# Optimization experiments

Measured on AMD Instinct MI355X. Metric: run time of the kernel, lower is better.

Reference implementation:

```python
import jax, jax.numpy as jnp
import numpy as np

B, N, T_OUT, C_IN, D_EMB, C_OUT = 8, 3072, 128, 32, 8, 64
BIG = 1e10


def setup_inputs() -> dict:
    key = jax.random.key(0)
    k = jax.random.split(key, 10)
    # x: (B, N, 3) tuples of (feature_id, value, time)
    f = jax.random.randint(k[0], (B, N), 0, C_IN).astype(jnp.float32)
    v = jax.random.normal(k[1], (B, N), dtype=jnp.float32)
    t = jax.random.uniform(k[2], (B, N), dtype=jnp.float32) * (T_OUT - 1)
    x = jnp.stack([f, v, t], axis=-1)
    out_positions = jnp.arange(T_OUT, dtype=jnp.float32)
    # parameters
    W_dist = jax.random.normal(k[3], (D_EMB,), dtype=jnp.float32) * 0.05   # Linear(1, D) weight
    b_dist = jnp.zeros((D_EMB,), dtype=jnp.float32)
    emb = jax.random.normal(k[4], (C_IN + 1, D_EMB), dtype=jnp.float32) * 0.05  # Embedding(C+1, D)
    W_vals = jax.random.normal(k[5], (D_EMB,), dtype=jnp.float32) * 0.05   # Linear(1, D) weight
    b_vals = jnp.zeros((D_EMB,), dtype=jnp.float32)
    W_lin = jax.random.normal(k[6], (C_OUT, D_EMB * C_IN), dtype=jnp.float32) * 0.05
    b_lin = jnp.zeros((C_OUT,), dtype=jnp.float32)
    kernel_scale = jnp.float32(0.5)
    return {"x": x, "out_positions": out_positions, "W_dist": W_dist, "b_dist": b_dist,
            "emb": emb, "W_vals": W_vals, "b_vals": b_vals, "W_lin": W_lin,
            "b_lin": b_lin, "kernel_scale": kernel_scale}


def reference(x, out_positions, W_dist, b_dist, emb, W_vals, b_vals, W_lin, b_lin, kernel_scale):
    C = emb.shape[0] - 1
    f = x[:, :, 0].astype(jnp.int32)   # (B, N) channel ids
    v = x[:, :, 1]                      # (B, N)
    t = x[:, :, 2]                      # (B, N)
    max_pos = jnp.max(out_positions)

    # --- observation encodings: (B, T, N, D) ---
    dists = (t[:, None, :] - out_positions[None, :, None]) / max_pos  # (B, T, N)
    x_enc = (dists[..., None] * W_dist + b_dist) \
            + emb[f][:, None, :, :] \
            + (v[:, :, None] * W_vals + b_vals)[:, None, :, :]

    # --- kernel inverse-density estimate (kernel_smoothing == 1 -> min), detached ---
    pd = jnp.abs(t[:, :, None] - t[:, None, :])          # (B, N, N)
    same = f[:, :, None] == f[:, None, :]
    pd = jnp.where(same & (pd != 0), pd, BIG)
    inv_density = jax.lax.stop_gradient(jnp.min(pd, axis=1))  # (B, N)

    # --- causal & padding masks ---
    causal = (t[:, None, :] - out_positions[None, :, None]) <= 0  # (B, T, N)
    padding = jnp.any(x != 0, axis=2)[:, None, :]                 # (B, 1, N)
    m = (causal & padding).astype(x.dtype)                        # (B, T, N)

    # --- per-channel density-weighted pooling, vectorized over channels ---
    # (density*mask)**ks == density**ks * mask since density>0 and mask in {0,1}
    dw = inv_density ** kernel_scale                              # (B, N)
    onehot = (f[:, :, None] == jnp.arange(C)).astype(x.dtype)     # (B, N, C)
    Z = jnp.einsum('btn,bn,bnc->btc', m, dw, onehot)              # density normalizer
    cnt = jnp.einsum('btn,bnc->btc', m, onehot)                   # mask count
    wx = x_enc * (m * dw[:, None, :])[..., None]                  # (B, T, N, D)
    num = jnp.einsum('btnd,bnc->btcd', wx, onehot)                # (B, T, C, D)
    fe = num / (Z + 1e-10)[..., None] / (cnt + 1e-10)[..., None]  # (B, T, C, D)

    y = fe.reshape(fe.shape[0], fe.shape[1], -1)                  # concat channels -> (B, T, C*D)
    out = y @ W_lin.T + b_lin                                     # (B, T, C_OUT)
    return jnp.transpose(out, (0, 2, 1))                          # (B, C_OUT, T)
```

## Files before the change

kernel.cpp:

```cpp
#include <hip/hip_runtime.h>
#include <math.h>

#define B 8
#define N 3072
#define T_OUTN 128
#define C_INN 32
#define D_EMBN 8
#define C_OUTN 64
#define BIGF 1e10f

__global__ void k12(const float* __restrict__ x,
                    const float* __restrict__ W_dist, const float* __restrict__ b_dist,
                    const float* __restrict__ emb,    const float* __restrict__ W_vals,
                    const float* __restrict__ b_vals, const float* __restrict__ W_lin,
                    const float* __restrict__ ks_p,
                    float* __restrict__ G, float* __restrict__ U) {
    const int tid = threadIdx.x;
    if (blockIdx.x == B * C_INN) {
        for (int e = tid; e < 3 * C_INN * C_OUTN; e += 256) {
            int comp = e / (C_INN * C_OUTN);
            int rem  = e % (C_INN * C_OUTN);
            int c = rem / C_OUTN;
            int o = rem % C_OUTN;
            float s = 0.f;
            #pragma unroll
            for (int d = 0; d < D_EMBN; ++d) {
                float w = W_lin[o * (C_INN * D_EMBN) + c * D_EMBN + d];
                float g;
                if (comp == 0)      g = W_dist[d];
                else if (comp == 1) g = b_dist[d] + b_vals[d] + emb[c * D_EMBN + d];
                else                g = W_vals[d];
                s += w * g;
            }
            U[e] = s;
        }
        return;
    }

    __shared__ __align__(16) float tl[N + 4];
    __shared__ float vl[N];
    __shared__ float hist[4][T_OUTN];
    __shared__ int cnt_s;

    const int b = blockIdx.x / C_INN;
    const int c = blockIdx.x % C_INN;
    const float* xb = x + (size_t)b * N * 3;

    for (int i = tid; i < 4 * T_OUTN; i += 256) ((float*)hist)[i] = 0.f;
    if (tid == 0) cnt_s = 0;
    __syncthreads();

    for (int idx = tid; idx < N; idx += 256) {
        float fv = xb[idx * 3 + 0];
        if ((int)fv == c) {
            float vv = xb[idx * 3 + 1];
            float tv = xb[idx * 3 + 2];
            int p = atomicAdd(&cnt_s, 1);
            tl[p] = tv;
            vl[p] = vv;
        }
    }
    __syncthreads();
    const int M = cnt_s;
    const int Mpad = (M + 3) & ~3;
    if (tid < Mpad - M) tl[M + tid] = -BIGF;
    __syncthreads();

    const float ks = ks_p[0];
    for (int p = tid; p < M; p += 256) {
        const float tp = tl[p];
        const float vp = vl[p];
        float m = BIGF;
        for (int j = 0; j < Mpad; j += 4) {
            float4 t4 = *(const float4*)&tl[j];
            float d0 = fabsf(t4.x - tp); if (d0 != 0.f) m = fminf(m, d0);
            float d1 = fabsf(t4.y - tp); if (d1 != 0.f) m = fminf(m, d1);
            float d2 = fabsf(t4.z - tp); if (d2 != 0.f) m = fminf(m, d2);
            float d3 = fabsf(t4.w - tp); if (d3 != 0.f) m = fminf(m, d3);
        }
        bool pad = (c == 0) && (tp == 0.f) && (vp == 0.f);
        if (!pad) {
            float w = powf(m, ks);
            int k = (int)ceilf(tp);
            atomicAdd(&hist[0][k], w);
            atomicAdd(&hist[1][k], 1.f);
            atomicAdd(&hist[2][k], w * tp);
            atomicAdd(&hist[3][k], w * vp);
        }
    }
    __syncthreads();

    {
        const int comp = tid >> 6;
        const int lane = tid & 63;
        float a  = hist[comp][2 * lane];
        float bb = hist[comp][2 * lane + 1];
        float s = a + bb;
        #pragma unroll
        for (int off = 1; off < 64; off <<= 1) {
            float t = __shfl_up(s, off);
            if (lane >= off) s += t;
        }
        hist[comp][2 * lane]     = s - bb;
        hist[comp][2 * lane + 1] = s;
    }
    __syncthreads();

    if (tid < T_OUTN) {
        const int tau = tid;
        float Z   = hist[0][tau];
        float cnt = hist[1][tau];
        float St  = hist[2][tau];
        float Sv  = hist[3][tau];
        float inv = 1.f / ((Z + 1e-10f) * (cnt + 1e-10f));
        float g1 = (St - (float)tau * Z) * inv * (1.f / 127.f);
        float g2 = Z * inv;
        float g3 = Sv * inv;
        float* Gb = G + (size_t)(b * C_INN + c) * 3 * T_OUTN;
        Gb[0 * T_OUTN + tau] = g1;
        Gb[1 * T_OUTN + tau] = g2;
        Gb[2 * T_OUTN + tau] = g3;
    }
}

__global__ void k3_out(const float* __restrict__ U, const float* __restrict__ G,
                       const float* __restrict__ b_lin, float* __restrict__ out) {
    __shared__ __align__(16) float Us[3 * C_INN * C_OUTN];
    __shared__ float Gs[4 * 100];
    const int tid = threadIdx.x;
    const int b  = blockIdx.x >> 5;
    const int t0 = (blockIdx.x & 31) * 4;

    for (int i = tid; i < (3 * C_INN * C_OUTN) / 4; i += 256)
        ((float4*)Us)[i] = ((const float4*)U)[i];
    for (int i = tid; i < 4 * C_INN * 3; i += 256) {
        int taul = i / (C_INN * 3);
        int rem  = i % (C_INN * 3);
        int c    = rem / 3;
        int comp = rem % 3;
        Gs[taul * 100 + rem] =
            G[((size_t)(b * C_INN + c) * 3 + comp) * T_OUTN + t0 + taul];
    }
    __syncthreads();

    const int o    = tid >> 2;
    const int taul = tid & 3;
    float acc = b_lin[o];
    #pragma unroll 4
    for (int c = 0; c < C_INN; ++c) {
        float g1 = Gs[taul * 100 + c * 3 + 0];
        float g2 = Gs[taul * 100 + c * 3 + 1];
        float g3 = Gs[taul * 100 + c * 3 + 2];
        acc += Us[0 * C_INN * C_OUTN + c * C_OUTN + o] * g1
             + Us[1 * C_INN * C_OUTN + c * C_OUTN + o] * g2
             + Us[2 * C_INN * C_OUTN + c * C_OUTN + o] * g3;
    }
    out[((size_t)b * C_OUTN + o) * T_OUTN + t0 + taul] = acc;
}

extern "C" void kernel_launch(void* const* d_in, const int* in_sizes, int n_in,
                              void* d_out, int out_size, void* d_ws, size_t ws_size,
                              hipStream_t stream) {
    const float* x      = (const float*)d_in[0];
    const float* W_dist = (const float*)d_in[2];
    const float* b_dist = (const float*)d_in[3];
    const float* emb    = (const float*)d_in[4];
    const float* W_vals = (const float*)d_in[5];
    const float* b_vals = (const float*)d_in[6];
    const float* W_lin  = (const float*)d_in[7];
    const float* b_lin  = (const float*)d_in[8];
    const float* ks     = (const float*)d_in[9];

    float* ws = (float*)d_ws;
    float* U  = ws;
    float* G  = U + 3 * C_INN * C_OUTN;
    float* out = (float*)d_out;

    k12<<<B * C_INN + 1, 256, 0, stream>>>(x, W_dist, b_dist, emb, W_vals,
                                           b_vals, W_lin, ks, G, U);
    k3_out<<<B * (T_OUTN / 4), 256, 0, stream>>>(U, G, b_lin, out);
}
```

Before: 103.2 us.

## Fuse both kernels into one per-batch block with channel-bucketed points

Replaces the two-kernel pipeline (one block per batch×channel, then a separate output projection kernel) with a single kernel of one 1024-thread block per batch. Points are counting-sorted by channel in shared memory, so each point scans only its own channel's bucket for the nearest-time distance. Per-channel histograms, the prefix sums, the projected weights and the final linear layer all stay in LDS, which removes the global workspace round trip and the second launch. The cost is only 8 blocks on a large GPU and heavy LDS use per block, so most CUs sit idle.

```diff
diff --git a/kernel.cpp b/kernel.cpp
--- a/kernel.cpp
+++ b/kernel.cpp
@@ -9,153 +9,131 @@
 #define C_OUTN 64
 #define BIGF 1e10f
 
-__global__ void k12(const float* __restrict__ x,
-                    const float* __restrict__ W_dist, const float* __restrict__ b_dist,
-                    const float* __restrict__ emb,    const float* __restrict__ W_vals,
-                    const float* __restrict__ b_vals, const float* __restrict__ W_lin,
-                    const float* __restrict__ ks_p,
-                    float* __restrict__ G, float* __restrict__ U) {
+__global__ __launch_bounds__(1024) void fused(
+    const float* __restrict__ x,
+    const float* __restrict__ W_dist, const float* __restrict__ b_dist,
+    const float* __restrict__ emb,    const float* __restrict__ W_vals,
+    const float* __restrict__ b_vals, const float* __restrict__ W_lin,
+    const float* __restrict__ b_lin,  const float* __restrict__ ks_p,
+    float* __restrict__ out)
+{
+    __shared__ __align__(16) float tl[N];
+    __shared__ float vl[N];
+    __shared__ int   cl[N];
+    __shared__ float hist[C_INN][4][T_OUTN];
+    __shared__ __align__(16) float Us[3][C_INN][C_OUTN];
+    __shared__ int cnt[C_INN], off[C_INN + 1], place[C_INN];
+
     const int tid = threadIdx.x;
-    if (blockIdx.x == B * C_INN) {
-        for (int e = tid; e < 3 * C_INN * C_OUTN; e += 256) {
-            int comp = e / (C_INN * C_OUTN);
-            int rem  = e % (C_INN * C_OUTN);
-            int c = rem / C_OUTN;
-            int o = rem % C_OUTN;
-            float s = 0.f;
-            #pragma unroll
-            for (int d = 0; d < D_EMBN; ++d) {
-                float w = W_lin[o * (C_INN * D_EMBN) + c * D_EMBN + d];
-                float g;
-                if (comp == 0)      g = W_dist[d];
-                else if (comp == 1) g = b_dist[d] + b_vals[d] + emb[c * D_EMBN + d];
-                else                g = W_vals[d];
-                s += w * g;
-            }
-            U[e] = s;
-        }
-        return;
-    }
-
-    __shared__ __align__(16) float tl[N + 4];
-    __shared__ float vl[N];
-    __shared__ float hist[4][T_OUTN];
-    __shared__ int cnt_s;
-
-    const int b = blockIdx.x / C_INN;
-    const int c = blockIdx.x % C_INN;
+    const int b   = blockIdx.x;
     const float* xb = x + (size_t)b * N * 3;
 
-    for (int i = tid; i < 4 * T_OUTN; i += 256) ((float*)hist)[i] = 0.f;
-    if (tid == 0) cnt_s = 0;
+    for (int i = tid; i < C_INN * 4 * T_OUTN; i += 1024) ((float*)hist)[i] = 0.f;
+    if (tid < C_INN) cnt[tid] = 0;
     __syncthreads();
 
-    for (int idx = tid; idx < N; idx += 256) {
-        float fv = xb[idx * 3 + 0];
-        if ((int)fv == c) {
-            float vv = xb[idx * 3 + 1];
-            float tv = xb[idx * 3 + 2];
-            int p = atomicAdd(&cnt_s, 1);
-            tl[p] = tv;
-            vl[p] = vv;
+    for (int i = tid; i < N; i += 1024) {
+        int c = (int)xb[i * 3];
+        atomicAdd(&cnt[c], 1);
+    }
+    for (int e = tid; e < 3 * C_INN * C_OUTN; e += 1024) {
+        int comp = e / (C_INN * C_OUTN);
+        int rem  = e % (C_INN * C_OUTN);
+        int c = rem / C_OUTN, o = rem % C_OUTN;
+        float s = 0.f;
+        #pragma unroll
+        for (int d = 0; d < D_EMBN; ++d) {
+            float w = W_lin[o * (C_INN * D_EMBN) + c * D_EMBN + d];
+            float g = (comp == 0) ? W_dist[d]
+                    : (comp == 1) ? (b_dist[d] + b_vals[d] + emb[c * D_EMBN + d])
+                    :               W_vals[d];
+            s += w * g;
         }
+        ((float*)Us)[e] = s;
     }
     __syncthreads();
-    const int M = cnt_s;
-    const int Mpad = (M + 3) & ~3;
-    if (tid < Mpad - M) tl[M + tid] = -BIGF;
+
+    if (tid == 0) {
+        int acc = 0;
+        for (int c = 0; c < C_INN; ++c) { off[c] = acc; place[c] = acc; acc += cnt[c]; }
+        off[C_INN] = acc;
+    }
+    __syncthreads();
+
+    for (int i = tid; i < N; i += 1024) {
+        int   c = (int)xb[i * 3];
+        float v = xb[i * 3 + 1];
+        float t = xb[i * 3 + 2];
+        int p = atomicAdd(&place[c], 1);
+        tl[p] = t; vl[p] = v; cl[p] = c;
+    }
     __syncthreads();
 
     const float ks = ks_p[0];
-    for (int p = tid; p < M; p += 256) {
+    for (int p = tid; p < N; p += 1024) {
+        const int   c  = cl[p];
         const float tp = tl[p];
         const float vp = vl[p];
+        const int j0 = off[c], j1 = off[c + 1];
         float m = BIGF;
-        for (int j = 0; j < Mpad; j += 4) {
-            float4 t4 = *(const float4*)&tl[j];
-            float d0 = fabsf(t4.x - tp); if (d0 != 0.f) m = fminf(m, d0);
-            float d1 = fabsf(t4.y - tp); if (d1 != 0.f) m = fminf(m, d1);
-            float d2 = fabsf(t4.z - tp); if (d2 != 0.f) m = fminf(m, d2);
-            float d3 = fabsf(t4.w - tp); if (d3 != 0.f) m = fminf(m, d3);
+        for (int j = j0; j < j1; ++j) {
+            float d = fabsf(tl[j] - tp);
+            if (d != 0.f) m = fminf(m, d);
         }
         bool pad = (c == 0) && (tp == 0.f) && (vp == 0.f);
         if (!pad) {
             float w = powf(m, ks);
             int k = (int)ceilf(tp);
-            atomicAdd(&hist[0][k], w);
-            atomicAdd(&hist[1][k], 1.f);
-            atomicAdd(&hist[2][k], w * tp);
-            atomicAdd(&hist[3][k], w * vp);
+            atomicAdd(&hist[c][0][k], w);
+            atomicAdd(&hist[c][1][k], 1.f);
+            atomicAdd(&hist[c][2][k], w * tp);
+            atomicAdd(&hist[c][3][k], w * vp);
         }
     }
     __syncthreads();
 
     {
-        const int comp = tid >> 6;
-        const int lane = tid & 63;
-        float a  = hist[comp][2 * lane];
-        float bb = hist[comp][2 * lane + 1];
-        float s = a + bb;
-        #pragma unroll
-        for (int off = 1; off < 64; off <<= 1) {
-            float t = __shfl_up(s, off);
-            if (lane >= off) s += t;
+        const int wv = tid >> 6, lane = tid & 63;
+        for (int s = wv; s < C_INN * 4; s += 16) {
+            float* h = &hist[s >> 2][s & 3][0];
+            float a  = h[2 * lane];
+            float bb = h[2 * lane + 1];
+            float sum = a + bb;
+            #pragma unroll
+            for (int o2 = 1; o2 < 64; o2 <<= 1) {
+                float t = __shfl_up(sum, o2);
+                if (lane >= o2) sum += t;
+            }
+            h[2 * lane]     = sum - bb;
+            h[2 * lane + 1] = sum;
         }
-        hist[comp][2 * lane]     = s - bb;
-        hist[comp][2 * lane + 1] = s;
     }
     __syncthreads();
 
-    if (tid < T_OUTN) {
-        const int tau = tid;
-        float Z   = hist[0][tau];
-        float cnt = hist[1][tau];
-        float St  = hist[2][tau];
-        float Sv  = hist[3][tau];
-        float inv = 1.f / ((Z + 1e-10f) * (cnt + 1e-10f));
-        float g1 = (St - (float)tau * Z) * inv * (1.f / 127.f);
-        float g2 = Z * inv;
-        float g3 = Sv * inv;
-        float* Gb = G + (size_t)(b * C_INN + c) * 3 * T_OUTN;
-        Gb[0 * T_OUTN + tau] = g1;
-        Gb[1 * T_OUTN + tau] = g2;
-        Gb[2 * T_OUTN + tau] = g3;
-    }
-}
-
-__global__ void k3_out(const float* __restrict__ U, const float* __restrict__ G,
-                       const float* __restrict__ b_lin, float* __restrict__ out) {
-    __shared__ __align__(16) float Us[3 * C_INN * C_OUTN];
-    __shared__ float Gs[4 * 100];
-    const int tid = threadIdx.x;
-    const int b  = blockIdx.x >> 5;
-    const int t0 = (blockIdx.x & 31) * 4;
-
-    for (int i = tid; i < (3 * C_INN * C_OUTN) / 4; i += 256)
-        ((float4*)Us)[i] = ((const float4*)U)[i];
-    for (int i = tid; i < 4 * C_INN * 3; i += 256) {
-        int taul = i / (C_INN * 3);
-        int rem  = i % (C_INN * 3);
-        int c    = rem / 3;
-        int comp = rem % 3;
-        Gs[taul * 100 + rem] =
-            G[((size_t)(b * C_INN + c) * 3 + comp) * T_OUTN + t0 + taul];
+    for (int e = tid; e < C_INN * T_OUTN; e += 1024) {
+        int c = e >> 7, tau = e & 127;
+        float Z  = hist[c][0][tau];
+        float ct = hist[c][1][tau];
+        float St = hist[c][2][tau];
+        float Sv = hist[c][3][tau];
+        float inv = 1.f / ((Z + 1e-10f) * (ct + 1e-10f));
+        hist[c][0][tau] = (St - (float)tau * Z) * inv * (1.f / 127.f);
+        hist[c][1][tau] = Z * inv;
+        hist[c][2][tau] = Sv * inv;
     }
     __syncthreads();
 
-    const int o    = tid >> 2;
-    const int taul = tid & 3;
-    float acc = b_lin[o];
-    #pragma unroll 4
-    for (int c = 0; c < C_INN; ++c) {
-        float g1 = Gs[taul * 100 + c * 3 + 0];
-        float g2 = Gs[taul * 100 + c * 3 + 1];
-        float g3 = Gs[taul * 100 + c * 3 + 2];
-        acc += Us[0 * C_INN * C_OUTN + c * C_OUTN + o] * g1
-             + Us[1 * C_INN * C_OUTN + c * C_OUTN + o] * g2
-             + Us[2 * C_INN * C_OUTN + c * C_OUTN + o] * g3;
+    for (int e = tid; e < C_OUTN * T_OUTN; e += 1024) {
+        int o = e >> 7, tau = e & 127;
+        float acc = b_lin[o];
+        #pragma unroll 4
+        for (int c = 0; c < C_INN; ++c) {
+            acc += Us[0][c][o] * hist[c][0][tau]
+                 + Us[1][c][o] * hist[c][1][tau]
+                 + Us[2][c][o] * hist[c][2][tau];
+        }
+        out[((size_t)b * C_OUTN + o) * T_OUTN + tau] = acc;
     }
-    out[((size_t)b * C_OUTN + o) * T_OUTN + t0 + taul] = acc;
 }
 
 extern "C" void kernel_launch(void* const* d_in, const int* in_sizes, int n_in,
@@ -171,12 +149,6 @@
     const float* b_lin  = (const float*)d_in[8];
     const float* ks     = (const float*)d_in[9];
 
-    float* ws = (float*)d_ws;
-    float* U  = ws;
-    float* G  = U + 3 * C_INN * C_OUTN;
-    float* out = (float*)d_out;
-
-    k12<<<B * C_INN + 1, 256, 0, stream>>>(x, W_dist, b_dist, emb, W_vals,
-                                           b_vals, W_lin, ks, G, U);
-    k3_out<<<B * (T_OUTN / 4), 256, 0, stream>>>(U, G, b_lin, out);
+    fused<<<B, 1024, 0, stream>>>(x, W_dist, b_dist, emb, W_vals, b_vals,
+                                  W_lin, b_lin, ks, (float*)d_out);
 }
```

Measured after the change: 150.7 us. +46.1%, slower.
